# Performance work log

Hardware: AMD Instinct MI355X
Metric: run time of the kernel (lower is better)

The kernel has to match this reference:

```python
import jax, jax.numpy as jnp
import numpy as np

ATOM = 34
HID = 256
LATENT = 128
CELLS = 512
B, N = 64, 128
NEG = -9e15


def setup_inputs() -> dict:
    key = jax.random.key(0)
    ks = jax.random.split(key, 20)
    inp = {}
    inp["xs"] = jax.random.normal(ks[0], (B, N, ATOM), dtype=jnp.float32)
    inp["A"] = jax.random.randint(ks[1], (B, N, N), 0, 2, dtype=jnp.int32)
    inp["cell_emb"] = jax.random.normal(ks[2], (B, CELLS), dtype=jnp.float32)
    inp["Wg"] = jax.random.normal(ks[3], (3, ATOM, ATOM), dtype=jnp.float32) * 0.17
    inp["bg"] = jnp.zeros((3, ATOM), dtype=jnp.float32)
    inp["attn"] = jax.random.normal(ks[4], (3, 2 * ATOM), dtype=jnp.float32) * 0.17
    # W_gnn_trans: 34 -> 256
    inp["Wt"] = jax.random.normal(ks[5], (ATOM, HID), dtype=jnp.float32) * 0.08
    inp["bt"] = jnp.zeros((HID,), dtype=jnp.float32)
    # ffn: 256 -> 34 ; ffn2: 34 -> latent
    inp["Wf"] = jax.random.normal(ks[6], (HID, ATOM), dtype=jnp.float32) * 0.08
    inp["bf"] = jnp.zeros((ATOM,), dtype=jnp.float32)
    inp["Wf2"] = jax.random.normal(ks[7], (ATOM, LATENT), dtype=jnp.float32) * 0.11
    inp["bf2"] = jnp.zeros((LATENT,), dtype=jnp.float32)
    # Decoder MLP: (latent+cells)->128->256->512->1
    din = LATENT + CELLS
    inp["W1"] = jax.random.normal(ks[8], (din, 128), dtype=jnp.float32) * 0.05
    inp["b1"] = jnp.zeros((128,), dtype=jnp.float32)
    inp["W2"] = jax.random.normal(ks[9], (128, 256), dtype=jnp.float32) * 0.07
    inp["b2"] = jnp.zeros((256,), dtype=jnp.float32)
    inp["W3"] = jax.random.normal(ks[10], (256, 512), dtype=jnp.float32) * 0.05
    inp["b3"] = jnp.zeros((512,), dtype=jnp.float32)
    inp["W4"] = jax.random.normal(ks[11], (512, 1), dtype=jnp.float32) * 0.06
    inp["b4"] = jnp.zeros((1,), dtype=jnp.float32)
    return inp


def reference(xs, A, cell_emb, Wg, bg, attn, Wt, bt, Wf, bf, Wf2, bf2,
              W1, b1, W2, b2, W3, b3, W4, b4):
    # ---- gnn(): 3 rounds of GAT-style masked-softmax message passing ----
    # a_input[b,p,q] = [h[b,p], h[b,q]], so e = leaky_relu(h@a1 outer+ h@a2)
    h0 = xs
    mask = A > 0  # [B,N,N]
    x = xs
    for i in range(3):
        h = jax.nn.relu(jnp.einsum('bnd,de->bne', x, Wg[i]) + bg[i])  # [B,N,34]
        f_src = h @ attn[i, :ATOM]   # [B,N] -- score contribution of row atom
        f_dst = h @ attn[i, ATOM:]   # [B,N] -- score contribution of col atom
        e = jax.nn.leaky_relu(f_src[:, :, None] + f_dst[:, None, :], 0.01)
        scores = jnp.where(mask, e, NEG)
        att = jax.nn.softmax(scores, axis=2)  # dropout disabled (deterministic)
        x = x + jnp.einsum('bpq,bqd->bpd', att, h)
    g = jax.nn.relu(jnp.einsum('bnd,dh->bnh', x, Wt) + bt)  # [B,N,HID]

    # ---- VEC_forward ----
    d = jnp.einsum('bnh,hd->bnd', g, Wf) + bf + h0        # ffn + residual to input xs
    d = jnp.einsum('bnd,dl->bnl', d, Wf2) + bf2           # [B,N,LATENT]
    d = jnp.max(d, axis=1)                                # [B,LATENT]
    vec = jax.nn.sigmoid(jnp.concatenate([d, cell_emb], axis=-1))

    # ---- Decoder_mlp (dropout disabled) ----
    hminus = jax.nn.relu(vec @ W1 + b1)
    hminus = jax.nn.relu(hminus @ W2 + b2)
    hminus = jax.nn.relu(hminus @ W3 + b3)
    score = hminus @ W4 + b4                              # [B,1]
    return score
```

## Files before the change

### kernel.cpp

```cpp
#include <hip/hip_runtime.h>

constexpr int ATOM = 34;
constexpr int HID = 256;
constexpr int LATENT = 128;
constexpr int CELLS = 512;
constexpr int NN = 128;
constexpr int NA = NN * ATOM;
#define NEGF (-9e15f)

__global__ __launch_bounds__(256, 2) void k_gat(
    const float* __restrict__ xsrc, const int* __restrict__ A,
    const float* __restrict__ Wg, const float* __restrict__ bg,
    const float* __restrict__ av, float* __restrict__ X)
{
    const int b = blockIdx.x >> 3, s8 = blockIdx.x & 7;
    const int t = threadIdx.x, lane = t & 63, wave = t >> 6;
    const int p0 = s8 * 16;

    __shared__ __align__(16) float xl[NN * 36];
    __shared__ __align__(16) float hlT[ATOM * 132];
    __shared__ __align__(16) float att[16 * NN];
    __shared__ __align__(16) float wgT[ATOM * 36];
    __shared__ float fs[NN], fd[NN], bgs[ATOM], avs[2 * ATOM];

    for (int i = t; i < ATOM * ATOM; i += 256) {
        int d = i / ATOM, e = i - d * ATOM;
        wgT[e * 36 + d] = Wg[i];
    }
    if (t < 68)  wgT[(t >> 1) * 36 + 34 + (t & 1)] = 0.f;
    if (t < ATOM)     bgs[t] = bg[t];
    if (t < 2 * ATOM) avs[t] = av[t];
    const float* xp = xsrc + b * NA;
    for (int i = t; i < NA; i += 256) xl[(i / ATOM) * 36 + (i % ATOM)] = xp[i];
    xl[(t >> 1) * 36 + 34 + (t & 1)] = 0.f;
    __syncthreads();

    {
        const int n = t >> 1, sub = t & 1;
        float xr[36];
        {
            float4* xr4 = (float4*)xr;
            const float4* p4 = (const float4*)(xl + n * 36);
            #pragma unroll
            for (int k = 0; k < 9; ++k) xr4[k] = p4[k];
        }
        #pragma unroll
        for (int j = 0; j < 17; ++j) {
            const int e = sub + 2 * j;
            float acc = bgs[e];
            const float4* wp = (const float4*)(wgT + e * 36);
            #pragma unroll
            for (int k = 0; k < 9; ++k) {
                float4 w = wp[k];
                acc += xr[4*k] * w.x + xr[4*k+1] * w.y + xr[4*k+2] * w.z + xr[4*k+3] * w.w;
            }
            hlT[e * 132 + n] = fmaxf(acc, 0.f);
        }
    }
    __syncthreads();

    {
        const int n = t & 127, w = t >> 7;
        const float* avp = avs + w * ATOM;
        float acc = 0.f;
        #pragma unroll
        for (int d = 0; d < ATOM; ++d) acc += hlT[d * 132 + n] * avp[d];
        if (w == 0) fs[n] = acc; else fd[n] = acc;
    }
    __syncthreads();

    const int* Ab = A + b * NN * NN;
    #pragma unroll
    for (int i = 0; i < 4; ++i) {
        int lp = wave * 4 + i, gp = p0 + lp;
        float fsv = fs[gp];
        unsigned long long m0 = __ballot(Ab[gp * NN + lane] > 0);
        unsigned long long m1 = __ballot(Ab[gp * NN + 64 + lane] > 0);
        float s0 = fsv + fd[lane];
        s0 = (s0 > 0.f) ? s0 : 0.01f * s0;
        if (!((m0 >> lane) & 1ull)) s0 = NEGF;
        float s1 = fsv + fd[64 + lane];
        s1 = (s1 > 0.f) ? s1 : 0.01f * s1;
        if (!((m1 >> lane) & 1ull)) s1 = NEGF;
        float mx = fmaxf(s0, s1);
        #pragma unroll
        for (int o = 32; o >= 1; o >>= 1) mx = fmaxf(mx, __shfl_xor(mx, o, 64));
        float e0 = __expf(s0 - mx), e1 = __expf(s1 - mx);
        float sm = e0 + e1;
        #pragma unroll
        for (int o = 32; o >= 1; o >>= 1) sm += __shfl_xor(sm, o, 64);
        float inv = 1.f / sm;
        att[lp * NN + lane]      = e0 * inv;
        att[lp * NN + 64 + lane] = e1 * inv;
    }
    __syncthreads();

    {
        const int p = t >> 4, g = t & 15, gp = p0 + p;
        const float4* ap  = (const float4*)(att + p * NN);
        const float4* h1p = (const float4*)(hlT + g * 132);
        const float4* h2p = (const float4*)(hlT + (g + 16) * 132);
        float a1 = 0.f, a2 = 0.f;
        #pragma unroll 8
        for (int k = 0; k < 32; ++k) {
            float4 a4 = ap[k], x1 = h1p[k], x2 = h2p[k];
            a1 += a4.x * x1.x + a4.y * x1.y + a4.z * x1.z + a4.w * x1.w;
            a2 += a4.x * x2.x + a4.y * x2.y + a4.z * x2.z + a4.w * x2.w;
        }
        float* Xr = X + b * NA + gp * ATOM;
        Xr[g]      = xl[gp * 36 + g] + a1;
        Xr[g + 16] = xl[gp * 36 + g + 16] + a2;
        if (g < 2) {
            const float4* h3p = (const float4*)(hlT + (g + 32) * 132);
            float a3 = 0.f;
            #pragma unroll 8
            for (int k = 0; k < 32; ++k) {
                float4 a4 = ap[k], x3 = h3p[k];
                a3 += a4.x * x3.x + a4.y * x3.y + a4.z * x3.z + a4.w * x3.w;
            }
            Xr[g + 32] = xl[gp * 36 + g + 32] + a3;
        }
    }
}

__global__ __launch_bounds__(512, 2) void k_phaseB(
    const float* __restrict__ X, const float* __restrict__ xs,
    const float* __restrict__ Wt, const float* __restrict__ bt,
    const float* __restrict__ Wf, const float* __restrict__ bf,
    const float* __restrict__ Wf2, const float* __restrict__ bf2,
    float* __restrict__ DM)
{
    const int b = blockIdx.x >> 2, q4 = blockIdx.x & 3;
    const int t = threadIdx.x;
    const int p0 = q4 * 32;
    __shared__ float wt[HID * 36];
    __shared__ float wf[HID * 36];
    __shared__ float xl[32][36];
    __shared__ float dlT[ATOM][33];
    __shared__ float wf2s[ATOM * LATENT];
    __shared__ float bts[HID];
    __shared__ float bfs[ATOM];
    __shared__ float sl[512];

    for (int i = t; i < ATOM * HID; i += 512) {
        int d = i >> 8, h = i & 255;
        wt[h * 36 + d] = Wt[i];
    }
    for (int i = t; i < HID * ATOM; i += 512) {
        int h = i / ATOM, j = i % ATOM;
        wf[h * 36 + j] = Wf[i];
    }
    for (int i = t; i < ATOM * LATENT; i += 512) wf2s[i] = Wf2[i];
    if (t < HID)  bts[t] = bt[t];
    if (t < ATOM) bfs[t] = bf[t];
    for (int i = t; i < 32 * ATOM; i += 512) xl[i / ATOM][i % ATOM] = X[b * NA + p0 * ATOM + i];
    __syncthreads();

    const int row = t & 31, sub = t >> 5;
    float dp[ATOM];
    #pragma unroll
    for (int j = 0; j < ATOM; ++j) dp[j] = 0.f;
    {
        float xr[36];
        float4* xr4 = (float4*)xr;
        const float4* xlr = (const float4*)&xl[row][0];
        #pragma unroll
        for (int k = 0; k < 9; ++k) xr4[k] = xlr[k];
        for (int i = 0; i < 16; ++i) {
            const int h = sub + 16 * i;
            float acc = bts[h];
            const float4* wtp = (const float4*)&wt[h * 36];
            #pragma unroll
            for (int k = 0; k < 8; ++k) {
                float4 w4 = wtp[k];
                acc += xr[4*k] * w4.x + xr[4*k+1] * w4.y + xr[4*k+2] * w4.z + xr[4*k+3] * w4.w;
            }
            acc += xr[32] * wt[h * 36 + 32] + xr[33] * wt[h * 36 + 33];
            acc = fmaxf(acc, 0.f);
            const float4* wfp = (const float4*)&wf[h * 36];
            #pragma unroll
            for (int k = 0; k < 8; ++k) {
                float4 w4 = wfp[k];
                dp[4*k]   += acc * w4.x; dp[4*k+1] += acc * w4.y;
                dp[4*k+2] += acc * w4.z; dp[4*k+3] += acc * w4.w;
            }
            dp[32] += acc * wf[h * 36 + 32];
            dp[33] += acc * wf[h * 36 + 33];
        }
    }
    __syncthreads();
    {
        float* pl = (sub < 8) ? wt : wf;
        const int s8 = sub & 7;
        #pragma unroll
        for (int j = 0; j < ATOM; ++j) pl[(s8 * 32 + row) * ATOM + j] = dp[j];
    }
    __syncthreads();
    for (int i = t; i < 32 * ATOM; i += 512) {
        int rr = i / ATOM, j = i % ATOM;
        float dv = bfs[j] + xs[b * NA + (p0 + rr) * ATOM + j];
        #pragma unroll
        for (int s = 0; s < 8; ++s)
            dv += wt[(s * 32 + rr) * ATOM + j] + wf[(s * 32 + rr) * ATOM + j];
        dlT[j][rr] = dv;
    }
    __syncthreads();
    {
        const int l = t & 127, chunk = t >> 7;
        float w2r[ATOM];
        #pragma unroll
        for (int j = 0; j < ATOM; ++j) w2r[j] = wf2s[j * LATENT + l];
        float mx = -3.4e38f;
        for (int rr = chunk * 8; rr < chunk * 8 + 8; ++rr) {
            float acc = bf2[l];
            #pragma unroll
            for (int j = 0; j < ATOM; ++j) acc += dlT[j][rr] * w2r[j];
            mx = fmaxf(mx, acc);
        }
        sl[chunk * 128 + l] = mx;
    }
    __syncthreads();
    if (t < LATENT)
        DM[(b * 4 + q4) * LATENT + t] =
            fmaxf(fmaxf(sl[t], sl[128 + t]), fmaxf(sl[256 + t], sl[384 + t]));
}

__global__ __launch_bounds__(1024) void k_dec(
    const float* __restrict__ DM, const float* __restrict__ cell,
    const float* __restrict__ W1, const float* __restrict__ b1,
    const float* __restrict__ W2, const float* __restrict__ b2,
    const float* __restrict__ W3, const float* __restrict__ b3,
    const float* __restrict__ W4, const float* __restrict__ b4,
    float* __restrict__ out)
{
    const int b = blockIdx.x, t = threadIdx.x, lane = t & 63, wave = t >> 6;
    __shared__ float vec[LATENT + CELLS];
    __shared__ float h1[128], h2[256], h3[512];
    __shared__ float sl[1024];
    if (t < LATENT) {
        float m = fmaxf(fmaxf(DM[(b*4+0)*LATENT + t], DM[(b*4+1)*LATENT + t]),
                        fmaxf(DM[(b*4+2)*LATENT + t], DM[(b*4+3)*LATENT + t]));
        vec[t] = 1.f / (1.f + __expf(-m));
    } else if (t >= 512) {
        int c = t - 512;
        vec[LATENT + c] = 1.f / (1.f + __expf(-cell[b * CELLS + c]));
    }
    __syncthreads();
    {
        const int j = t & 127, part = t >> 7;
        float acc = 0.f;
        #pragma unroll 4
        for (int k = part * 80; k < part * 80 + 80; ++k)
            acc += vec[k] * W1[k * 128 + j];
        sl[part * 128 + j] = acc;
    }
    __syncthreads();
    if (t < 128) {
        float v = b1[t];
        #pragma unroll
        for (int p = 0; p < 8; ++p) v += sl[p * 128 + t];
        h1[t] = fmaxf(v, 0.f);
    }
    __syncthreads();
    {
        const int j = t & 255, part = t >> 8;
        float acc = 0.f;
        #pragma unroll 4
        for (int k = part * 32; k < part * 32 + 32; ++k)
            acc += h1[k] * W2[k * 256 + j];
        sl[part * 256 + j] = acc;
    }
    __syncthreads();
    if (t < 256) h2[t] = fmaxf(sl[t] + sl[256 + t] + sl[512 + t] + sl[768 + t] + b2[t], 0.f);
    __syncthreads();
    {
        const int j = t & 511, part = t >> 9;
        float acc = 0.f;
        #pragma unroll 4
        for (int k = part * 128; k < part * 128 + 128; ++k)
            acc += h2[k] * W3[k * 512 + j];
        sl[part * 512 + j] = acc;
    }
    __syncthreads();
    if (t < 512) h3[t] = fmaxf(sl[t] + sl[512 + t] + b3[t], 0.f);
    __syncthreads();
    float v = (t < 512) ? h3[t] * W4[t] : 0.f;
    #pragma unroll
    for (int o = 32; o >= 1; o >>= 1) v += __shfl_xor(v, o, 64);
    if (lane == 0) sl[wave] = v;
    __syncthreads();
    if (t == 0) {
        float s = b4[0];
        #pragma unroll
        for (int w = 0; w < 16; ++w) s += sl[w];
        out[b] = s;
    }
}

extern "C" void kernel_launch(void* const* d_in, const int* in_sizes, int n_in,
                              void* d_out, int out_size, void* d_ws, size_t ws_size,
                              hipStream_t stream) {
    const float* xs       = (const float*)d_in[0];
    const int*   A        = (const int*)  d_in[1];
    const float* cell_emb = (const float*)d_in[2];
    const float* Wg       = (const float*)d_in[3];
    const float* bg       = (const float*)d_in[4];
    const float* attnv    = (const float*)d_in[5];
    const float* Wt       = (const float*)d_in[6];
    const float* bt       = (const float*)d_in[7];
    const float* Wf       = (const float*)d_in[8];
    const float* bf       = (const float*)d_in[9];
    const float* Wf2      = (const float*)d_in[10];
    const float* bf2      = (const float*)d_in[11];
    const float* W1       = (const float*)d_in[12];
    const float* b1       = (const float*)d_in[13];
    const float* W2       = (const float*)d_in[14];
    const float* b2       = (const float*)d_in[15];
    const float* W3       = (const float*)d_in[16];
    const float* b3       = (const float*)d_in[17];
    const float* W4       = (const float*)d_in[18];
    const float* b4       = (const float*)d_in[19];
    float* out = (float*)d_out;

    float* W  = (float*)d_ws;
    float* X0 = W;
    float* X1 = W + 278528;
    float* DM = W + 557056;

    k_gat<<<512, 256, 0, stream>>>(xs, A, Wg,                   bg,            attnv,           X0);
    k_gat<<<512, 256, 0, stream>>>(X0, A, Wg + ATOM * ATOM,     bg + ATOM,     attnv + 2*ATOM,  X1);
    k_gat<<<512, 256, 0, stream>>>(X1, A, Wg + 2 * ATOM * ATOM, bg + 2 * ATOM, attnv + 4*ATOM,  X0);
    k_phaseB<<<256, 512, 0, stream>>>(X0, xs, Wt, bt, Wf, bf, Wf2, bf2, DM);
    k_dec<<<64, 1024, 0, stream>>>(DM, cell_emb, W1, b1, W2, b2, W3, b3, W4, b4, out);
}
```

Measured before the change: 177.8 us.

## Fuse all stages into one cooperative megakernel with grid syncs

```diff
diff --git a/kernel.cpp b/kernel.cpp
--- a/kernel.cpp
+++ b/kernel.cpp
@@ -1,4 +1,6 @@
 #include <hip/hip_runtime.h>
+#include <hip/hip_cooperative_groups.h>
+namespace cg = cooperative_groups;
 
 constexpr int ATOM = 34;
 constexpr int HID = 256;
@@ -8,291 +10,322 @@
 constexpr int NA = NN * ATOM;
 #define NEGF (-9e15f)
 
-__global__ __launch_bounds__(256, 2) void k_gat(
-    const float* __restrict__ xsrc, const int* __restrict__ A,
-    const float* __restrict__ Wg, const float* __restrict__ bg,
-    const float* __restrict__ av, float* __restrict__ X)
-{
-    const int b = blockIdx.x >> 3, s8 = blockIdx.x & 7;
-    const int t = threadIdx.x, lane = t & 63, wave = t >> 6;
-    const int p0 = s8 * 16;
-
-    __shared__ __align__(16) float xl[NN * 36];
-    __shared__ __align__(16) float hlT[ATOM * 132];
-    __shared__ __align__(16) float att[16 * NN];
-    __shared__ __align__(16) float wgT[ATOM * 36];
-    __shared__ float fs[NN], fd[NN], bgs[ATOM], avs[2 * ATOM];
-
-    for (int i = t; i < ATOM * ATOM; i += 256) {
-        int d = i / ATOM, e = i - d * ATOM;
-        wgT[e * 36 + d] = Wg[i];
-    }
-    if (t < 68)  wgT[(t >> 1) * 36 + 34 + (t & 1)] = 0.f;
-    if (t < ATOM)     bgs[t] = bg[t];
-    if (t < 2 * ATOM) avs[t] = av[t];
-    const float* xp = xsrc + b * NA;
-    for (int i = t; i < NA; i += 256) xl[(i / ATOM) * 36 + (i % ATOM)] = xp[i];
-    xl[(t >> 1) * 36 + 34 + (t & 1)] = 0.f;
-    __syncthreads();
-
-    {
-        const int n = t >> 1, sub = t & 1;
-        float xr[36];
-        {
-            float4* xr4 = (float4*)xr;
-            const float4* p4 = (const float4*)(xl + n * 36);
-            #pragma unroll
-            for (int k = 0; k < 9; ++k) xr4[k] = p4[k];
-        }
-        #pragma unroll
-        for (int j = 0; j < 17; ++j) {
-            const int e = sub + 2 * j;
-            float acc = bgs[e];
-            const float4* wp = (const float4*)(wgT + e * 36);
-            #pragma unroll
-            for (int k = 0; k < 9; ++k) {
-                float4 w = wp[k];
-                acc += xr[4*k] * w.x + xr[4*k+1] * w.y + xr[4*k+2] * w.z + xr[4*k+3] * w.w;
-            }
-            hlT[e * 132 + n] = fmaxf(acc, 0.f);
-        }
-    }
-    __syncthreads();
-
-    {
-        const int n = t & 127, w = t >> 7;
-        const float* avp = avs + w * ATOM;
-        float acc = 0.f;
-        #pragma unroll
-        for (int d = 0; d < ATOM; ++d) acc += hlT[d * 132 + n] * avp[d];
-        if (w == 0) fs[n] = acc; else fd[n] = acc;
-    }
-    __syncthreads();
-
-    const int* Ab = A + b * NN * NN;
-    #pragma unroll
-    for (int i = 0; i < 4; ++i) {
-        int lp = wave * 4 + i, gp = p0 + lp;
-        float fsv = fs[gp];
-        unsigned long long m0 = __ballot(Ab[gp * NN + lane] > 0);
-        unsigned long long m1 = __ballot(Ab[gp * NN + 64 + lane] > 0);
-        float s0 = fsv + fd[lane];
-        s0 = (s0 > 0.f) ? s0 : 0.01f * s0;
-        if (!((m0 >> lane) & 1ull)) s0 = NEGF;
-        float s1 = fsv + fd[64 + lane];
-        s1 = (s1 > 0.f) ? s1 : 0.01f * s1;
-        if (!((m1 >> lane) & 1ull)) s1 = NEGF;
-        float mx = fmaxf(s0, s1);
-        #pragma unroll
-        for (int o = 32; o >= 1; o >>= 1) mx = fmaxf(mx, __shfl_xor(mx, o, 64));
-        float e0 = __expf(s0 - mx), e1 = __expf(s1 - mx);
-        float sm = e0 + e1;
-        #pragma unroll
-        for (int o = 32; o >= 1; o >>= 1) sm += __shfl_xor(sm, o, 64);
-        float inv = 1.f / sm;
-        att[lp * NN + lane]      = e0 * inv;
-        att[lp * NN + 64 + lane] = e1 * inv;
-    }
-    __syncthreads();
-
-    {
-        const int p = t >> 4, g = t & 15, gp = p0 + p;
-        const float4* ap  = (const float4*)(att + p * NN);
-        const float4* h1p = (const float4*)(hlT + g * 132);
-        const float4* h2p = (const float4*)(hlT + (g + 16) * 132);
-        float a1 = 0.f, a2 = 0.f;
-        #pragma unroll 8
-        for (int k = 0; k < 32; ++k) {
-            float4 a4 = ap[k], x1 = h1p[k], x2 = h2p[k];
-            a1 += a4.x * x1.x + a4.y * x1.y + a4.z * x1.z + a4.w * x1.w;
-            a2 += a4.x * x2.x + a4.y * x2.y + a4.z * x2.z + a4.w * x2.w;
-        }
-        float* Xr = X + b * NA + gp * ATOM;
-        Xr[g]      = xl[gp * 36 + g] + a1;
-        Xr[g + 16] = xl[gp * 36 + g + 16] + a2;
-        if (g < 2) {
-            const float4* h3p = (const float4*)(hlT + (g + 32) * 132);
-            float a3 = 0.f;
-            #pragma unroll 8
-            for (int k = 0; k < 32; ++k) {
-                float4 a4 = ap[k], x3 = h3p[k];
-                a3 += a4.x * x3.x + a4.y * x3.y + a4.z * x3.z + a4.w * x3.w;
-            }
-            Xr[g + 32] = xl[gp * 36 + g + 32] + a3;
-        }
-    }
-}
-
-__global__ __launch_bounds__(512, 2) void k_phaseB(
-    const float* __restrict__ X, const float* __restrict__ xs,
+constexpr int P_XL   = 0;
+constexpr int P_HLT  = 4608;
+constexpr int P_ATT  = 9096;
+constexpr int P_MASK = 13320;
+constexpr int P_FS   = 13448;
+constexpr int P_FD   = 13576;
+constexpr int P_WT   = 0;
+constexpr int P_WF   = 9216;
+constexpr int P_DLT  = 18432;
+constexpr int P_SL   = 19554;
+constexpr int P_XQ   = 20100;
+constexpr int P_VEC  = 0;
+constexpr int P_DSL  = 640;
+constexpr int P_H1   = 1152;
+constexpr int P_H2   = 1280;
+constexpr int POOL   = 21252;
+
+__global__ __launch_bounds__(512, 2) void mega(
+    const float* __restrict__ xs, const int* __restrict__ A,
+    const float* __restrict__ cell,
+    const float* __restrict__ Wg3, const float* __restrict__ bg3,
+    const float* __restrict__ av3,
     const float* __restrict__ Wt, const float* __restrict__ bt,
     const float* __restrict__ Wf, const float* __restrict__ bf,
     const float* __restrict__ Wf2, const float* __restrict__ bf2,
-    float* __restrict__ DM)
-{
-    const int b = blockIdx.x >> 2, q4 = blockIdx.x & 3;
-    const int t = threadIdx.x;
-    const int p0 = q4 * 32;
-    __shared__ float wt[HID * 36];
-    __shared__ float wf[HID * 36];
-    __shared__ float xl[32][36];
-    __shared__ float dlT[ATOM][33];
-    __shared__ float wf2s[ATOM * LATENT];
-    __shared__ float bts[HID];
-    __shared__ float bfs[ATOM];
-    __shared__ float sl[512];
-
-    for (int i = t; i < ATOM * HID; i += 512) {
-        int d = i >> 8, h = i & 255;
-        wt[h * 36 + d] = Wt[i];
-    }
-    for (int i = t; i < HID * ATOM; i += 512) {
-        int h = i / ATOM, j = i % ATOM;
-        wf[h * 36 + j] = Wf[i];
-    }
-    for (int i = t; i < ATOM * LATENT; i += 512) wf2s[i] = Wf2[i];
-    if (t < HID)  bts[t] = bt[t];
-    if (t < ATOM) bfs[t] = bf[t];
-    for (int i = t; i < 32 * ATOM; i += 512) xl[i / ATOM][i % ATOM] = X[b * NA + p0 * ATOM + i];
-    __syncthreads();
-
-    const int row = t & 31, sub = t >> 5;
-    float dp[ATOM];
-    #pragma unroll
-    for (int j = 0; j < ATOM; ++j) dp[j] = 0.f;
-    {
-        float xr[36];
-        float4* xr4 = (float4*)xr;
-        const float4* xlr = (const float4*)&xl[row][0];
-        #pragma unroll
-        for (int k = 0; k < 9; ++k) xr4[k] = xlr[k];
-        for (int i = 0; i < 16; ++i) {
-            const int h = sub + 16 * i;
-            float acc = bts[h];
-            const float4* wtp = (const float4*)&wt[h * 36];
-            #pragma unroll
-            for (int k = 0; k < 8; ++k) {
-                float4 w4 = wtp[k];
-                acc += xr[4*k] * w4.x + xr[4*k+1] * w4.y + xr[4*k+2] * w4.z + xr[4*k+3] * w4.w;
-            }
-            acc += xr[32] * wt[h * 36 + 32] + xr[33] * wt[h * 36 + 33];
-            acc = fmaxf(acc, 0.f);
-            const float4* wfp = (const float4*)&wf[h * 36];
-            #pragma unroll
-            for (int k = 0; k < 8; ++k) {
-                float4 w4 = wfp[k];
-                dp[4*k]   += acc * w4.x; dp[4*k+1] += acc * w4.y;
-                dp[4*k+2] += acc * w4.z; dp[4*k+3] += acc * w4.w;
-            }
-            dp[32] += acc * wf[h * 36 + 32];
-            dp[33] += acc * wf[h * 36 + 33];
-        }
-    }
-    __syncthreads();
-    {
-        float* pl = (sub < 8) ? wt : wf;
-        const int s8 = sub & 7;
-        #pragma unroll
-        for (int j = 0; j < ATOM; ++j) pl[(s8 * 32 + row) * ATOM + j] = dp[j];
-    }
-    __syncthreads();
-    for (int i = t; i < 32 * ATOM; i += 512) {
-        int rr = i / ATOM, j = i % ATOM;
-        float dv = bfs[j] + xs[b * NA + (p0 + rr) * ATOM + j];
-        #pragma unroll
-        for (int s = 0; s < 8; ++s)
-            dv += wt[(s * 32 + rr) * ATOM + j] + wf[(s * 32 + rr) * ATOM + j];
-        dlT[j][rr] = dv;
-    }
-    __syncthreads();
-    {
-        const int l = t & 127, chunk = t >> 7;
-        float w2r[ATOM];
-        #pragma unroll
-        for (int j = 0; j < ATOM; ++j) w2r[j] = wf2s[j * LATENT + l];
-        float mx = -3.4e38f;
-        for (int rr = chunk * 8; rr < chunk * 8 + 8; ++rr) {
-            float acc = bf2[l];
-            #pragma unroll
-            for (int j = 0; j < ATOM; ++j) acc += dlT[j][rr] * w2r[j];
-            mx = fmaxf(mx, acc);
-        }
-        sl[chunk * 128 + l] = mx;
-    }
-    __syncthreads();
-    if (t < LATENT)
-        DM[(b * 4 + q4) * LATENT + t] =
-            fmaxf(fmaxf(sl[t], sl[128 + t]), fmaxf(sl[256 + t], sl[384 + t]));
-}
-
-__global__ __launch_bounds__(1024) void k_dec(
-    const float* __restrict__ DM, const float* __restrict__ cell,
     const float* __restrict__ W1, const float* __restrict__ b1,
     const float* __restrict__ W2, const float* __restrict__ b2,
     const float* __restrict__ W3, const float* __restrict__ b3,
     const float* __restrict__ W4, const float* __restrict__ b4,
-    float* __restrict__ out)
+    float* __restrict__ out, float* __restrict__ X0, float* __restrict__ X1,
+    float* __restrict__ DM)
 {
-    const int b = blockIdx.x, t = threadIdx.x, lane = t & 63, wave = t >> 6;
-    __shared__ float vec[LATENT + CELLS];
-    __shared__ float h1[128], h2[256], h3[512];
-    __shared__ float sl[1024];
+    cg::grid_group grid = cg::this_grid();
+    __shared__ __align__(16) float pool[POOL];
+    const int bid = blockIdx.x, b = bid >> 2, q4 = bid & 3;
+    const int t = threadIdx.x, lane = t & 63, wave = t >> 6;
+    const int p0 = q4 * 32;
+
+    float* xl  = pool + P_XL;
+    float* hlT = pool + P_HLT;
+    float* att = pool + P_ATT;
+    unsigned long long* mask = (unsigned long long*)(pool + P_MASK);
+    float* fs  = pool + P_FS;
+    float* fd  = pool + P_FD;
+    float* xq  = pool + P_XQ;
+
+    const int halfU = __builtin_amdgcn_readfirstlane(t >> 7);
+    const int waveU = __builtin_amdgcn_readfirstlane(wave);
+    const int nIdx  = t & 127;
+
+    if (t < 256) xl[(t >> 1) * 36 + 34 + (t & 1)] = 0.f;
+
+    for (int r = 0; r < 3; ++r) {
+        const float* Wgr = Wg3 + r * ATOM * ATOM;
+        const float* bgr = bg3 + r * ATOM;
+        const float* avr = av3 + r * 2 * ATOM;
+        const float* xsrc = (r == 0) ? (xs + b * NA) : (((r == 1) ? X0 : X1) + b * NA);
+
+        for (int i = t; i < NA; i += 512) xl[(i / ATOM) * 36 + (i % ATOM)] = xsrc[i];
+        __syncthreads();
+
+        {
+            float xr[36];
+            {
+                float4* x4 = (float4*)xr;
+                const float4* p4 = (const float4*)(xl + nIdx * 36);
+                #pragma unroll
+                for (int k = 0; k < 9; ++k) x4[k] = p4[k];
+            }
+            #pragma unroll
+            for (int j = 0; j < 9; ++j) {
+                const int e = halfU * 9 + j;
+                if (e < ATOM) {
+                    float acc = bgr[e];
+                    #pragma unroll
+                    for (int d = 0; d < ATOM; ++d) acc += xr[d] * Wgr[d * ATOM + e];
+                    hlT[e * 132 + nIdx] = fmaxf(acc, 0.f);
+                }
+            }
+        }
+        __syncthreads();
+
+        if (halfU < 2) {
+            const float* avp = avr + halfU * ATOM;
+            float acc = 0.f;
+            #pragma unroll
+            for (int d = 0; d < ATOM; ++d) acc += hlT[d * 132 + nIdx] * avp[d];
+            if (halfU == 0) fs[nIdx] = acc; else fd[nIdx] = acc;
+        }
+        __syncthreads();
+
+        const int* Ab = A + b * NN * NN;
+        #pragma unroll
+        for (int i = 0; i < 4; ++i) {
+            const int lp = wave * 4 + i, gp = p0 + lp;
+            unsigned long long m0, m1;
+            if (r == 0) {
+                m0 = __ballot(Ab[gp * NN + lane] > 0);
+                m1 = __ballot(Ab[gp * NN + 64 + lane] > 0);
+                if (lane == 0) { mask[lp * 2] = m0; mask[lp * 2 + 1] = m1; }
+            } else {
+                m0 = mask[lp * 2]; m1 = mask[lp * 2 + 1];
+            }
+            float fsv = fs[gp];
+            float s0 = fsv + fd[lane];
+            s0 = (s0 > 0.f) ? s0 : 0.01f * s0;
+            if (!((m0 >> lane) & 1ull)) s0 = NEGF;
+            float s1 = fsv + fd[64 + lane];
+            s1 = (s1 > 0.f) ? s1 : 0.01f * s1;
+            if (!((m1 >> lane) & 1ull)) s1 = NEGF;
+            float mx = fmaxf(s0, s1);
+            #pragma unroll
+            for (int o = 32; o >= 1; o >>= 1) mx = fmaxf(mx, __shfl_xor(mx, o, 64));
+            float e0 = __expf(s0 - mx), e1 = __expf(s1 - mx);
+            float sm = e0 + e1;
+            #pragma unroll
+            for (int o = 32; o >= 1; o >>= 1) sm += __shfl_xor(sm, o, 64);
+            float inv = 1.f / sm;
+            att[lp * 132 + lane]      = e0 * inv;
+            att[lp * 132 + 64 + lane] = e1 * inv;
+        }
+        __syncthreads();
+
+        {
+            const int p = t >> 4, g = t & 15, gp = p0 + p;
+            const float4* ap  = (const float4*)(att + p * 132);
+            const float4* h1p = (const float4*)(hlT + g * 132);
+            const float4* h2p = (const float4*)(hlT + (g + 16) * 132);
+            float a1 = 0.f, a2 = 0.f;
+            #pragma unroll 8
+            for (int k = 0; k < 32; ++k) {
+                float4 a4 = ap[k], x1 = h1p[k], x2 = h2p[k];
+                a1 += a4.x * x1.x + a4.y * x1.y + a4.z * x1.z + a4.w * x1.w;
+                a2 += a4.x * x2.x + a4.y * x2.y + a4.z * x2.z + a4.w * x2.w;
+            }
+            float a3 = 0.f;
+            if (g < 2) {
+                const float4* h3p = (const float4*)(hlT + (g + 32) * 132);
+                #pragma unroll 8
+                for (int k = 0; k < 32; ++k) {
+                    float4 a4 = ap[k], x3 = h3p[k];
+                    a3 += a4.x * x3.x + a4.y * x3.y + a4.z * x3.z + a4.w * x3.w;
+                }
+            }
+            if (r < 2) {
+                float* Xr = ((r == 0) ? X0 : X1) + b * NA + gp * ATOM;
+                Xr[g]      = xl[gp * 36 + g] + a1;
+                Xr[g + 16] = xl[gp * 36 + g + 16] + a2;
+                if (g < 2) Xr[g + 32] = xl[gp * 36 + g + 32] + a3;
+            } else {
+                xq[p * 36 + g]      = xl[gp * 36 + g] + a1;
+                xq[p * 36 + g + 16] = xl[gp * 36 + g + 16] + a2;
+                if (g < 2) {
+                    xq[p * 36 + g + 32] = xl[gp * 36 + g + 32] + a3;
+                    xq[p * 36 + 34 + g] = 0.f;
+                }
+            }
+        }
+        if (r < 2) grid.sync();
+    }
+    __syncthreads();
+
+    float* wt  = pool + P_WT;
+    float* wf  = pool + P_WF;
+    float* pl  = pool + P_WT;
+    float* dlT = pool + P_DLT;
+    float* sl  = pool + P_SL;
+
+    for (int i = t; i < ATOM * HID; i += 512) {
+        int d = i >> 8, h = i & 255;
+        wt[h * 36 + d] = Wt[i];
+    }
+    for (int i = t; i < HID * ATOM; i += 512) {
+        int h = i / ATOM, j = i - (i / ATOM) * ATOM;
+        wf[h * 36 + j] = Wf[i];
+    }
+    wt[(t >> 1) * 36 + 34 + (t & 1)] = 0.f;
+    wf[(t >> 1) * 36 + 34 + (t & 1)] = 0.f;
+    __syncthreads();
+
+    {
+        const int rp = t & 15, sub = t >> 4, s2 = (lane >> 4);
+        float xrA[36], xrB[36], dpA[36], dpB[36];
+        {
+            float4* a4 = (float4*)xrA; float4* b4v = (float4*)xrB;
+            const float4* pa = (const float4*)(xq + rp * 36);
+            const float4* pb = (const float4*)(xq + (rp + 16) * 36);
+            #pragma unroll
+            for (int k = 0; k < 9; ++k) { a4[k] = pa[k]; b4v[k] = pb[k]; }
+        }
+        #pragma unroll
+        for (int j = 0; j < 36; ++j) { dpA[j] = 0.f; dpB[j] = 0.f; }
+        #pragma unroll
+        for (int i = 0; i < 8; ++i) {
+            const int h = sub + 32 * i;
+            const float4* wtp = (const float4*)(wt + h * 36);
+            float a = 0.f, c = 0.f;
+            #pragma unroll
+            for (int k = 0; k < 9; ++k) {
+                float4 w4 = wtp[k];
+                a += xrA[4*k] * w4.x + xrA[4*k+1] * w4.y + xrA[4*k+2] * w4.z + xrA[4*k+3] * w4.w;
+                c += xrB[4*k] * w4.x + xrB[4*k+1] * w4.y + xrB[4*k+2] * w4.z + xrB[4*k+3] * w4.w;
+            }
+            const float btv = bt[h];
+            const float gA = fmaxf(a + btv, 0.f), gB = fmaxf(c + btv, 0.f);
+            const float4* wfp = (const float4*)(wf + h * 36);
+            #pragma unroll
+            for (int k = 0; k < 9; ++k) {
+                float4 w4 = wfp[k];
+                dpA[4*k]   += gA * w4.x; dpA[4*k+1] += gA * w4.y;
+                dpA[4*k+2] += gA * w4.z; dpA[4*k+3] += gA * w4.w;
+                dpB[4*k]   += gB * w4.x; dpB[4*k+1] += gB * w4.y;
+                dpB[4*k+2] += gB * w4.z; dpB[4*k+3] += gB * w4.w;
+            }
+        }
+        __syncthreads();
+        #pragma unroll
+        for (int j = 0; j < ATOM; ++j) {
+            float a = dpA[j];
+            a += __shfl_xor(a, 16, 64); a += __shfl_xor(a, 32, 64);
+            float c = dpB[j];
+            c += __shfl_xor(c, 16, 64); c += __shfl_xor(c, 32, 64);
+            if (s2 == 0) {
+                pl[(waveU * 32 + rp) * ATOM + j]      = a;
+                pl[(waveU * 32 + rp + 16) * ATOM + j] = c;
+            }
+        }
+    }
+    __syncthreads();
+
+    {
+        const float* xsq = xs + b * NA + p0 * ATOM;
+        for (int i = t; i < 32 * ATOM; i += 512) {
+            int rr = i / ATOM, j = i - rr * ATOM;
+            float dv = bf[j] + xsq[rr * ATOM + j];
+            #pragma unroll
+            for (int w = 0; w < 8; ++w) dv += pl[(w * 32 + rr) * ATOM + j];
+            dlT[j * 33 + rr] = dv;
+        }
+    }
+    __syncthreads();
+
+    {
+        const int l = t & 127, chunk = t >> 7;
+        float w2r[ATOM];
+        #pragma unroll
+        for (int j = 0; j < ATOM; ++j) w2r[j] = Wf2[j * LATENT + l];
+        const float bb = bf2[l];
+        float mx = -3.4e38f;
+        #pragma unroll
+        for (int r8 = 0; r8 < 8; ++r8) {
+            const int rr = chunk * 8 + r8;
+            float acc = bb;
+            #pragma unroll
+            for (int j = 0; j < ATOM; ++j) acc += dlT[j * 33 + rr] * w2r[j];
+            mx = fmaxf(mx, acc);
+        }
+        sl[chunk * 128 + l] = mx;
+    }
+    __syncthreads();
+    if (t < LATENT)
+        DM[(b * 4 + q4) * LATENT + t] =
+            fmaxf(fmaxf(sl[t], sl[128 + t]), fmaxf(sl[256 + t], sl[384 + t]));
+
+    grid.sync();
+
+    if (q4 != 0) return;
+    float* vec = pool + P_VEC;
+    float* dsl = pool + P_DSL;
+    float* h1  = pool + P_H1;
+    float* h2  = pool + P_H2;
+
     if (t < LATENT) {
         float m = fmaxf(fmaxf(DM[(b*4+0)*LATENT + t], DM[(b*4+1)*LATENT + t]),
                         fmaxf(DM[(b*4+2)*LATENT + t], DM[(b*4+3)*LATENT + t]));
         vec[t] = 1.f / (1.f + __expf(-m));
-    } else if (t >= 512) {
-        int c = t - 512;
-        vec[LATENT + c] = 1.f / (1.f + __expf(-cell[b * CELLS + c]));
-    }
+    }
+    vec[LATENT + t] = 1.f / (1.f + __expf(-cell[b * CELLS + t]));
     __syncthreads();
     {
         const int j = t & 127, part = t >> 7;
         float acc = 0.f;
-        #pragma unroll 4
-        for (int k = part * 80; k < part * 80 + 80; ++k)
+        #pragma unroll 8
+        for (int k = part * 160; k < part * 160 + 160; ++k)
             acc += vec[k] * W1[k * 128 + j];
-        sl[part * 128 + j] = acc;
-    }
-    __syncthreads();
-    if (t < 128) {
-        float v = b1[t];
-        #pragma unroll
-        for (int p = 0; p < 8; ++p) v += sl[p * 128 + t];
-        h1[t] = fmaxf(v, 0.f);
-    }
-    __syncthreads();
-    {
-        const int j = t & 255, part = t >> 8;
+        dsl[part * 128 + j] = acc;
+    }
+    __syncthreads();
+    if (t < 128)
+        h1[t] = fmaxf(dsl[t] + dsl[128 + t] + dsl[256 + t] + dsl[384 + t] + b1[t], 0.f);
+    __syncthreads();
+    {
+        const int j = t & 255, half = t >> 8;
         float acc = 0.f;
-        #pragma unroll 4
-        for (int k = part * 32; k < part * 32 + 32; ++k)
+        #pragma unroll 8
+        for (int k = half * 64; k < half * 64 + 64; ++k)
             acc += h1[k] * W2[k * 256 + j];
-        sl[part * 256 + j] = acc;
-    }
-    __syncthreads();
-    if (t < 256) h2[t] = fmaxf(sl[t] + sl[256 + t] + sl[512 + t] + sl[768 + t] + b2[t], 0.f);
-    __syncthreads();
-    {
-        const int j = t & 511, part = t >> 9;
-        float acc = 0.f;
-        #pragma unroll 4
-        for (int k = part * 128; k < part * 128 + 128; ++k)
-            acc += h2[k] * W3[k * 512 + j];
-        sl[part * 512 + j] = acc;
-    }
-    __syncthreads();
-    if (t < 512) h3[t] = fmaxf(sl[t] + sl[512 + t] + b3[t], 0.f);
-    __syncthreads();
-    float v = (t < 512) ? h3[t] * W4[t] : 0.f;
-    #pragma unroll
-    for (int o = 32; o >= 1; o >>= 1) v += __shfl_xor(v, o, 64);
-    if (lane == 0) sl[wave] = v;
+        dsl[half * 256 + j] = acc;
+    }
+    __syncthreads();
+    if (t < 256) h2[t] = fmaxf(dsl[t] + dsl[256 + t] + b2[t], 0.f);
+    __syncthreads();
+    {
+        float acc = b3[t];
+        #pragma unroll 8
+        for (int k = 0; k < 256; ++k) acc += h2[k] * W3[k * 512 + t];
+        float v = fmaxf(acc, 0.f) * W4[t];
+        #pragma unroll
+        for (int o = 32; o >= 1; o >>= 1) v += __shfl_xor(v, o, 64);
+        if (lane == 0) dsl[wave] = v;
+    }
     __syncthreads();
     if (t == 0) {
         float s = b4[0];
         #pragma unroll
-        for (int w = 0; w < 16; ++w) s += sl[w];
+        for (int w = 0; w < 8; ++w) s += dsl[w];
         out[b] = s;
     }
 }
@@ -322,14 +355,19 @@
     const float* b4       = (const float*)d_in[19];
     float* out = (float*)d_out;
 
-    float* W  = (float*)d_ws;
-    float* X0 = W;
-    float* X1 = W + 278528;
-    float* DM = W + 557056;
-
-    k_gat<<<512, 256, 0, stream>>>(xs, A, Wg,                   bg,            attnv,           X0);
-    k_gat<<<512, 256, 0, stream>>>(X0, A, Wg + ATOM * ATOM,     bg + ATOM,     attnv + 2*ATOM,  X1);
-    k_gat<<<512, 256, 0, stream>>>(X1, A, Wg + 2 * ATOM * ATOM, bg + 2 * ATOM, attnv + 4*ATOM,  X0);
-    k_phaseB<<<256, 512, 0, stream>>>(X0, xs, Wt, bt, Wf, bf, Wf2, bf2, DM);
-    k_dec<<<64, 1024, 0, stream>>>(DM, cell_emb, W1, b1, W2, b2, W3, b3, W4, b4, out);
+    float* Wsp = (float*)d_ws;
+    float* X0 = Wsp;
+    float* X1 = Wsp + 278528;
+    float* DM = Wsp + 557056;
+
+    void* kargs[] = {
+        (void*)&xs, (void*)&A, (void*)&cell_emb,
+        (void*)&Wg, (void*)&bg, (void*)&attnv,
+        (void*)&Wt, (void*)&bt, (void*)&Wf, (void*)&bf,
+        (void*)&Wf2, (void*)&bf2,
+        (void*)&W1, (void*)&b1, (void*)&W2, (void*)&b2,
+        (void*)&W3, (void*)&b3, (void*)&W4, (void*)&b4,
+        (void*)&out, (void*)&X0, (void*)&X1, (void*)&DM
+    };
+    hipLaunchCooperativeKernel((void*)mega, dim3(256), dim3(512), kargs, 0, stream);
 }
```

After: 296.8 us. +66.9%, slower.

## Precompute adjacency bitmasks and transposed GAT weights; restructure phaseB register tiling

Applied to the files above, without the earlier changes.

```diff
diff --git a/kernel.cpp b/kernel.cpp
--- a/kernel.cpp
+++ b/kernel.cpp
@@ -8,10 +8,33 @@
 constexpr int NA = NN * ATOM;
 #define NEGF (-9e15f)
 
+__global__ __launch_bounds__(256) void k_prep(
+    const int* __restrict__ A, const float* __restrict__ Wg3,
+    unsigned long long* __restrict__ M, float* __restrict__ WgT3)
+{
+    const int blk = blockIdx.x, t = threadIdx.x, lane = t & 63, wave = t >> 6;
+    if (blk < 64) {
+        const int* Ab = A + blk * NN * NN;
+        unsigned long long* Mb = M + blk * NN * 2;
+        for (int i = 0; i < 32; ++i) {
+            const int row = wave * 32 + i;
+            unsigned long long m0 = __ballot(Ab[row * NN + lane] > 0);
+            unsigned long long m1 = __ballot(Ab[row * NN + 64 + lane] > 0);
+            if (lane == 0) { Mb[row * 2] = m0; Mb[row * 2 + 1] = m1; }
+        }
+    } else {
+        for (int i = t; i < 3 * ATOM * 36; i += 256) {
+            const int r = i / (ATOM * 36), rem = i - r * ATOM * 36;
+            const int e = rem / 36, d = rem - e * 36;
+            WgT3[i] = (d < ATOM) ? Wg3[r * ATOM * ATOM + d * ATOM + e] : 0.f;
+        }
+    }
+}
+
 __global__ __launch_bounds__(256, 2) void k_gat(
-    const float* __restrict__ xsrc, const int* __restrict__ A,
-    const float* __restrict__ Wg, const float* __restrict__ bg,
-    const float* __restrict__ av, float* __restrict__ X)
+    const float* __restrict__ xsrc, const unsigned long long* __restrict__ M,
+    const float* __restrict__ WgTr, const float* __restrict__ bgr,
+    const float* __restrict__ avr, float* __restrict__ X)
 {
     const int b = blockIdx.x >> 3, s8 = blockIdx.x & 7;
     const int t = threadIdx.x, lane = t & 63, wave = t >> 6;
@@ -19,41 +42,31 @@
 
     __shared__ __align__(16) float xl[NN * 36];
     __shared__ __align__(16) float hlT[ATOM * 132];
-    __shared__ __align__(16) float att[16 * NN];
-    __shared__ __align__(16) float wgT[ATOM * 36];
-    __shared__ float fs[NN], fd[NN], bgs[ATOM], avs[2 * ATOM];
-
-    for (int i = t; i < ATOM * ATOM; i += 256) {
-        int d = i / ATOM, e = i - d * ATOM;
-        wgT[e * 36 + d] = Wg[i];
-    }
-    if (t < 68)  wgT[(t >> 1) * 36 + 34 + (t & 1)] = 0.f;
-    if (t < ATOM)     bgs[t] = bg[t];
-    if (t < 2 * ATOM) avs[t] = av[t];
+    __shared__ __align__(16) float att[16 * 132];
+    __shared__ float fs[NN], fd[NN];
+
     const float* xp = xsrc + b * NA;
     for (int i = t; i < NA; i += 256) xl[(i / ATOM) * 36 + (i % ATOM)] = xp[i];
     xl[(t >> 1) * 36 + 34 + (t & 1)] = 0.f;
     __syncthreads();
 
     {
-        const int n = t >> 1, sub = t & 1;
+        const int n = t & 127;
+        const int eh = __builtin_amdgcn_readfirstlane(t >> 7);
         float xr[36];
         {
-            float4* xr4 = (float4*)xr;
+            float4* x4 = (float4*)xr;
             const float4* p4 = (const float4*)(xl + n * 36);
             #pragma unroll
-            for (int k = 0; k < 9; ++k) xr4[k] = p4[k];
+            for (int k = 0; k < 9; ++k) x4[k] = p4[k];
         }
         #pragma unroll
         for (int j = 0; j < 17; ++j) {
-            const int e = sub + 2 * j;
-            float acc = bgs[e];
-            const float4* wp = (const float4*)(wgT + e * 36);
-            #pragma unroll
-            for (int k = 0; k < 9; ++k) {
-                float4 w = wp[k];
-                acc += xr[4*k] * w.x + xr[4*k+1] * w.y + xr[4*k+2] * w.z + xr[4*k+3] * w.w;
-            }
+            const int e = eh * 17 + j;
+            const float* wp = WgTr + e * 36;
+            float acc = bgr[e];
+            #pragma unroll
+            for (int d = 0; d < ATOM; ++d) acc += xr[d] * wp[d];
             hlT[e * 132 + n] = fmaxf(acc, 0.f);
         }
     }
@@ -61,7 +74,7 @@
 
     {
         const int n = t & 127, w = t >> 7;
-        const float* avp = avs + w * ATOM;
+        const float* avp = avr + w * ATOM;
         float acc = 0.f;
         #pragma unroll
         for (int d = 0; d < ATOM; ++d) acc += hlT[d * 132 + n] * avp[d];
@@ -69,13 +82,13 @@
     }
     __syncthreads();
 
-    const int* Ab = A + b * NN * NN;
+    const unsigned long long* Mb = M + b * NN * 2;
     #pragma unroll
     for (int i = 0; i < 4; ++i) {
-        int lp = wave * 4 + i, gp = p0 + lp;
-        float fsv = fs[gp];
-        unsigned long long m0 = __ballot(Ab[gp * NN + lane] > 0);
-        unsigned long long m1 = __ballot(Ab[gp * NN + 64 + lane] > 0);
+        const int lp = wave * 4 + i, gp = p0 + lp;
+        const unsigned long long m0 = Mb[gp * 2];
+        const unsigned long long m1 = Mb[gp * 2 + 1];
+        const float fsv = fs[gp];
         float s0 = fsv + fd[lane];
         s0 = (s0 > 0.f) ? s0 : 0.01f * s0;
         if (!((m0 >> lane) & 1ull)) s0 = NEGF;
@@ -90,14 +103,14 @@
         #pragma unroll
         for (int o = 32; o >= 1; o >>= 1) sm += __shfl_xor(sm, o, 64);
         float inv = 1.f / sm;
-        att[lp * NN + lane]      = e0 * inv;
-        att[lp * NN + 64 + lane] = e1 * inv;
+        att[lp * 132 + lane]      = e0 * inv;
+        att[lp * 132 + 64 + lane] = e1 * inv;
     }
     __syncthreads();
 
     {
         const int p = t >> 4, g = t & 15, gp = p0 + p;
-        const float4* ap  = (const float4*)(att + p * NN);
+        const float4* ap  = (const float4*)(att + p * 132);
         const float4* h1p = (const float4*)(hlT + g * 132);
         const float4* h2p = (const float4*)(hlT + (g + 16) * 132);
         float a1 = 0.f, a2 = 0.f;
@@ -123,7 +136,7 @@
     }
 }
 
-__global__ __launch_bounds__(512, 2) void k_phaseB(
+__global__ __launch_bounds__(512, 1) void k_phaseB(
     const float* __restrict__ X, const float* __restrict__ xs,
     const float* __restrict__ Wt, const float* __restrict__ bt,
     const float* __restrict__ Wf, const float* __restrict__ bf,
@@ -131,15 +144,12 @@
     float* __restrict__ DM)
 {
     const int b = blockIdx.x >> 2, q4 = blockIdx.x & 3;
-    const int t = threadIdx.x;
+    const int t = threadIdx.x, lane = t & 63, wave = t >> 6;
     const int p0 = q4 * 32;
-    __shared__ float wt[HID * 36];
-    __shared__ float wf[HID * 36];
-    __shared__ float xl[32][36];
-    __shared__ float dlT[ATOM][33];
-    __shared__ float wf2s[ATOM * LATENT];
-    __shared__ float bts[HID];
-    __shared__ float bfs[ATOM];
+    __shared__ __align__(16) float wt[HID * 36];
+    __shared__ __align__(16) float wf[HID * 36];
+    __shared__ __align__(16) float xl[32 * 36];
+    __shared__ float dlT[ATOM * 33];
     __shared__ float sl[512];
 
     for (int i = t; i < ATOM * HID; i += 512) {
@@ -147,74 +157,93 @@
         wt[h * 36 + d] = Wt[i];
     }
     for (int i = t; i < HID * ATOM; i += 512) {
-        int h = i / ATOM, j = i % ATOM;
+        int h = i / ATOM, j = i - (i / ATOM) * ATOM;
         wf[h * 36 + j] = Wf[i];
     }
-    for (int i = t; i < ATOM * LATENT; i += 512) wf2s[i] = Wf2[i];
-    if (t < HID)  bts[t] = bt[t];
-    if (t < ATOM) bfs[t] = bf[t];
-    for (int i = t; i < 32 * ATOM; i += 512) xl[i / ATOM][i % ATOM] = X[b * NA + p0 * ATOM + i];
-    __syncthreads();
-
-    const int row = t & 31, sub = t >> 5;
-    float dp[ATOM];
-    #pragma unroll
-    for (int j = 0; j < ATOM; ++j) dp[j] = 0.f;
-    {
-        float xr[36];
-        float4* xr4 = (float4*)xr;
-        const float4* xlr = (const float4*)&xl[row][0];
-        #pragma unroll
-        for (int k = 0; k < 9; ++k) xr4[k] = xlr[k];
-        for (int i = 0; i < 16; ++i) {
-            const int h = sub + 16 * i;
-            float acc = bts[h];
-            const float4* wtp = (const float4*)&wt[h * 36];
-            #pragma unroll
-            for (int k = 0; k < 8; ++k) {
+    wt[(t >> 1) * 36 + 34 + (t & 1)] = 0.f;
+    wf[(t >> 1) * 36 + 34 + (t & 1)] = 0.f;
+    for (int i = t; i < 32 * ATOM; i += 512) xl[(i / ATOM) * 36 + (i % ATOM)] = X[b * NA + p0 * ATOM + i];
+    if (t < 64) xl[(t >> 1) * 36 + 34 + (t & 1)] = 0.f;
+    __syncthreads();
+
+    const int waveU = __builtin_amdgcn_readfirstlane(wave);
+    {
+        const int rp = t & 15, sub = t >> 4, s2 = lane >> 4;
+        float xrA[36], xrB[36], dpA[36], dpB[36];
+        {
+            float4* a4 = (float4*)xrA; float4* b4v = (float4*)xrB;
+            const float4* pa = (const float4*)(xl + rp * 36);
+            const float4* pb = (const float4*)(xl + (rp + 16) * 36);
+            #pragma unroll
+            for (int k = 0; k < 9; ++k) { a4[k] = pa[k]; b4v[k] = pb[k]; }
+        }
+        #pragma unroll
+        for (int j = 0; j < 36; ++j) { dpA[j] = 0.f; dpB[j] = 0.f; }
+        #pragma unroll
+        for (int i = 0; i < 8; ++i) {
+            const int h = sub + 32 * i;
+            const float4* wtp = (const float4*)(wt + h * 36);
+            float a = 0.f, c = 0.f;
+            #pragma unroll
+            for (int k = 0; k < 9; ++k) {
                 float4 w4 = wtp[k];
-                acc += xr[4*k] * w4.x + xr[4*k+1] * w4.y + xr[4*k+2] * w4.z + xr[4*k+3] * w4.w;
+                a += xrA[4*k] * w4.x + xrA[4*k+1] * w4.y + xrA[4*k+2] * w4.z + xrA[4*k+3] * w4.w;
+                c += xrB[4*k] * w4.x + xrB[4*k+1] * w4.y + xrB[4*k+2] * w4.z + xrB[4*k+3] * w4.w;
             }
-            acc += xr[32] * wt[h * 36 + 32] + xr[33] * wt[h * 36 + 33];
-            acc = fmaxf(acc, 0.f);
-            const float4* wfp = (const float4*)&wf[h * 36];
-            #pragma unroll
-            for (int k = 0; k < 8; ++k) {
+            const float btv = bt[h];
+            const float gA = fmaxf(a + btv, 0.f), gB = fmaxf(c + btv, 0.f);
+            const float4* wfp = (const float4*)(wf + h * 36);
+            #pragma unroll
+            for (int k = 0; k < 9; ++k) {
                 float4 w4 = wfp[k];
-                dp[4*k]   += acc * w4.x; dp[4*k+1] += acc * w4.y;
-                dp[4*k+2] += acc * w4.z; dp[4*k+3] += acc * w4.w;
+                dpA[4*k]   += gA * w4.x; dpA[4*k+1] += gA * w4.y;
+                dpA[4*k+2] += gA * w4.z; dpA[4*k+3] += gA * w4.w;
+                dpB[4*k]   += gB * w4.x; dpB[4*k+1] += gB * w4.y;
+                dpB[4*k+2] += gB * w4.z; dpB[4*k+3] += gB * w4.w;
             }
-            dp[32] += acc * wf[h * 36 + 32];
-            dp[33] += acc * wf[h * 36 + 33];
-        }
-    }
-    __syncthreads();
-    {
-        float* pl = (sub < 8) ? wt : wf;
-        const int s8 = sub & 7;
-        #pragma unroll
-        for (int j = 0; j < ATOM; ++j) pl[(s8 * 32 + row) * ATOM + j] = dp[j];
-    }
-    __syncthreads();
-    for (int i = t; i < 32 * ATOM; i += 512) {
-        int rr = i / ATOM, j = i % ATOM;
-        float dv = bfs[j] + xs[b * NA + (p0 + rr) * ATOM + j];
-        #pragma unroll
-        for (int s = 0; s < 8; ++s)
-            dv += wt[(s * 32 + rr) * ATOM + j] + wf[(s * 32 + rr) * ATOM + j];
-        dlT[j][rr] = dv;
-    }
-    __syncthreads();
+        }
+        __syncthreads();
+        float* pl = wt;
+        #pragma unroll
+        for (int j = 0; j < ATOM; ++j) {
+            float a = dpA[j];
+            a += __shfl_xor(a, 16, 64); a += __shfl_xor(a, 32, 64);
+            float c = dpB[j];
+            c += __shfl_xor(c, 16, 64); c += __shfl_xor(c, 32, 64);
+            if (s2 == 0) {
+                pl[(waveU * 32 + rp) * ATOM + j]      = a;
+                pl[(waveU * 32 + rp + 16) * ATOM + j] = c;
+            }
+        }
+    }
+    __syncthreads();
+
+    {
+        float* pl = wt;
+        const float* xsq = xs + b * NA + p0 * ATOM;
+        for (int i = t; i < 32 * ATOM; i += 512) {
+            int rr = i / ATOM, j = i - rr * ATOM;
+            float dv = bf[j] + xsq[rr * ATOM + j];
+            #pragma unroll
+            for (int w = 0; w < 8; ++w) dv += pl[(w * 32 + rr) * ATOM + j];
+            dlT[j * 33 + rr] = dv;
+        }
+    }
+    __syncthreads();
+
     {
         const int l = t & 127, chunk = t >> 7;
         float w2r[ATOM];
         #pragma unroll
-        for (int j = 0; j < ATOM; ++j) w2r[j] = wf2s[j * LATENT + l];
+        for (int j = 0; j < ATOM; ++j) w2r[j] = Wf2[j * LATENT + l];
+        const float bb = bf2[l];
         float mx = -3.4e38f;
-        for (int rr = chunk * 8; rr < chunk * 8 + 8; ++rr) {
-            float acc = bf2[l];
-            #pragma unroll
-            for (int j = 0; j < ATOM; ++j) acc += dlT[j][rr] * w2r[j];
+        #pragma unroll
+        for (int r8 = 0; r8 < 8; ++r8) {
+            const int rr = chunk * 8 + r8;
+            float acc = bb;
+            #pragma unroll
+            for (int j = 0; j < ATOM; ++j) acc += dlT[j * 33 + rr] * w2r[j];
             mx = fmaxf(mx, acc);
         }
         sl[chunk * 128 + l] = mx;
@@ -322,14 +351,17 @@
     const float* b4       = (const float*)d_in[19];
     float* out = (float*)d_out;
 
-    float* W  = (float*)d_ws;
-    float* X0 = W;
-    float* X1 = W + 278528;
-    float* DM = W + 557056;
-
-    k_gat<<<512, 256, 0, stream>>>(xs, A, Wg,                   bg,            attnv,           X0);
-    k_gat<<<512, 256, 0, stream>>>(X0, A, Wg + ATOM * ATOM,     bg + ATOM,     attnv + 2*ATOM,  X1);
-    k_gat<<<512, 256, 0, stream>>>(X1, A, Wg + 2 * ATOM * ATOM, bg + 2 * ATOM, attnv + 4*ATOM,  X0);
+    float* Wsp = (float*)d_ws;
+    float* X0   = Wsp;
+    float* X1   = Wsp + 278528;
+    float* DM   = Wsp + 557056;
+    unsigned long long* Mm = (unsigned long long*)(Wsp + 589824);
+    float* WgT3 = Wsp + 622592;
+
+    k_prep<<<65, 256, 0, stream>>>(A, Wg, Mm, WgT3);
+    k_gat<<<512, 256, 0, stream>>>(xs, Mm, WgT3,        bg,      attnv,           X0);
+    k_gat<<<512, 256, 0, stream>>>(X0, Mm, WgT3 + 1224, bg + 34, attnv + 68,      X1);
+    k_gat<<<512, 256, 0, stream>>>(X1, Mm, WgT3 + 2448, bg + 68, attnv + 136,     X0);
     k_phaseB<<<256, 512, 0, stream>>>(X0, xs, Wt, bt, Wf, bf, Wf2, bf2, DM);
     k_dec<<<64, 1024, 0, stream>>>(DM, cell_emb, W1, b1, W2, b2, W3, b3, W4, b4, out);
 }
```

Result: slower. 208.2 us (+17.1%).
